# Kernel tuning notes

Measured on AMD Instinct MI355X. Metric: run time of the kernel, lower is better.

## Reference

```python
import jax, jax.numpy as jnp
import numpy as np

T, B, D = 2048, 2, 768
N, HD = 12, 64  # num_heads, head_dim; N*HD == D


def _rel_shift(s):
    # s: [I, J, B, N] -> Transformer-XL relative shift along J
    I, J, b, n = s.shape
    s = jnp.pad(s, ((0, 0), (1, 0), (0, 0), (0, 0)))  # [I, J+1, B, N]
    s = s.reshape(J + 1, I, b, n)[1:]                  # drop first row after transpose-view
    return s.reshape(I, J, b, n)


def setup_inputs() -> dict:
    key = jax.random.key(0)
    ks = jax.random.split(key, 8)
    x = jax.random.normal(ks[0], (T, B, D), dtype=jnp.float32)
    pos_encodings = jax.random.normal(ks[1], (T, D), dtype=jnp.float32)
    u_bias = jax.random.normal(ks[2], (N, HD), dtype=jnp.float32) * 0.02
    v_bias = jax.random.normal(ks[3], (N, HD), dtype=jnp.float32) * 0.02
    # causal mask: True = masked (j > i)
    attn_mask = jnp.triu(jnp.ones((T, T), dtype=bool), k=1)
    W_qkv = jax.random.normal(ks[4], (D, 3 * N * HD), dtype=jnp.float32) * 0.02
    W_pos = jax.random.normal(ks[5], (D, N * HD), dtype=jnp.float32) * 0.02
    W_out = jax.random.normal(ks[6], (N * HD, D), dtype=jnp.float32) * 0.02
    return {"x": x, "pos_encodings": pos_encodings, "u_bias": u_bias,
            "v_bias": v_bias, "W_qkv": W_qkv, "W_pos": W_pos,
            "W_out": W_out, "attn_mask": attn_mask}


def reference(x, pos_encodings, u_bias, v_bias, W_qkv, W_pos, W_out, attn_mask):
    tgt, bsz, dim = x.shape
    n, hd = u_bias.shape
    scale = 1.0 / (dim ** 0.5)  # NOTE: original scales by 1/sqrt(dim), not head_dim

    qkv = x @ W_qkv                                   # [T, B, 3*N*HD]
    q, k, v = jnp.split(qkv, 3, axis=-1)
    q = q.reshape(tgt, bsz, n, hd)
    k = k.reshape(tgt, bsz, n, hd)
    v = v.reshape(tgt, bsz, n, hd)
    pos = (pos_encodings @ W_pos).reshape(-1, n, hd)  # [P, N, HD]

    content_score = jnp.einsum('ibnd,jbnd->ijbn', q + u_bias, k)
    pos_score = jnp.einsum('ibnd,jnd->ijbn', q + v_bias, pos)
    pos_score = _rel_shift(pos_score)

    attn_score = (content_score + pos_score) * scale  # [T, S, B, N]
    attn_score = jnp.where(attn_mask[:, :, None, None], -jnp.inf, attn_score)
    attn = jax.nn.softmax(attn_score, axis=1)

    context = jnp.einsum('ijbn,jbnd->ibnd', attn, v)
    context = context.reshape(tgt, bsz, n * hd)
    return context @ W_out                            # [T, B, D]
```

## Files before the change

kernel.cpp:

```cpp
#include <hip/hip_runtime.h>
#include <math.h>

#define T_SEQ 2048
#define BSZ   2
#define DIM   768
#define NH    12
#define SCALE_L2 0.05205877f

typedef float f32x4 __attribute__((ext_vector_type(4)));
typedef __bf16 bf16x8 __attribute__((ext_vector_type(8)));
typedef unsigned int uint_t;
typedef unsigned short us16;

static __device__ __forceinline__ f32x4 mfma16(bf16x8 a, bf16x8 b, f32x4 c) {
    return __builtin_amdgcn_mfma_f32_16x16x32_bf16(a, b, c, 0, 0, 0);
}
static __device__ __forceinline__ us16 f2bf(float f) {
    uint_t u = __builtin_bit_cast(uint_t, f);
    u += 0x7fff + ((u >> 16) & 1);
    return (us16)(u >> 16);
}
static __device__ __forceinline__ us16 f2bf_up(float f) {
    return (us16)((__builtin_bit_cast(uint_t, f) + 0x8000u) >> 16);
}
static __device__ __forceinline__ float bf2f(us16 h) {
    return __builtin_bit_cast(float, (uint_t)h << 16);
}
static __device__ __forceinline__ bf16x8 ld_frag(const us16* p) {
    union { uint4 u; bf16x8 b; } x;
    x.u = *(const uint4*)p;
    return x.b;
}

typedef __attribute__((address_space(1))) const unsigned int guint;
typedef __attribute__((address_space(3))) unsigned int luint;
static __device__ __forceinline__ void glds16(const us16* g, us16* l) {
    __builtin_amdgcn_global_load_lds((guint*)g, (luint*)l, 16, 0, 0);
}

__constant__ int SLOT_IB[30] = {15,15,15, 14,14,14, 13,13, 12,12, 11,11,
                                10,10, 9,9, 8,8, 7,7, 6,6, 5, 4, 3,3, 2,2, 1, 0};
__constant__ int SLOT_C0[30] = {0,11,22, 0,10,20, 0,14, 0,13, 0,12,
                                0,11, 0,10, 0,14, 0,14, 0,12, 0, 0, 0,4, 0,3, 0, 0};
__constant__ int SLOT_C1[30] = {11,22,32, 10,20,30, 14,28, 13,26, 12,24,
                                11,22, 10,20, 14,18, 14,16, 12,14, 12, 10, 4,8, 3,6, 4, 2};
__constant__ int ORDER[30] = {6,7,16,18, 8,9, 10,11,20,22, 0,1,12,13,
                              2,3,4,5,14,15,23,
                              17,24,25,28, 26,27, 19,21,29};
__constant__ int CB_IB[12]   = {2,3,6,7,8,9,10,11,12,13,14,15};
__constant__ int CB_BASE[12] = {26,24,20,18,16,14,12,10,8,6,3,0};
__constant__ int CB_N[12]    = {2,2,2,2,2,2,2,2,2,2,3,3};

__global__ __launch_bounds__(256)
void cvt_all(const float* __restrict__ x, us16* __restrict__ xb, int n0,
             const float* __restrict__ pe, us16* __restrict__ peb, int n1,
             const float* __restrict__ w0, us16* __restrict__ o0,
             const float* __restrict__ w1, us16* __restrict__ o1,
             const float* __restrict__ w2, us16* __restrict__ o2) {
    const int bid = blockIdx.x;
    const int tid = threadIdx.x;
    if (bid < 1024) {
        int idx = bid * 256 + tid;
        int stride = 1024 * 256;
        int ntot = n0 + n1;
        for (int i = idx; i < ntot; i += stride) {
            const float4* src;
            ushort4* dst;
            if (i < n0) { src = (const float4*)x + i; dst = (ushort4*)xb + i; }
            else        { src = (const float4*)pe + (i - n0); dst = (ushort4*)peb + (i - n0); }
            float4 f = *src;
            ushort4 o;
            o.x = f2bf(f.x); o.y = f2bf(f.y); o.z = f2bf(f.z); o.w = f2bf(f.w);
            *dst = o;
        }
        return;
    }
    __shared__ us16 Ts[64][72];
    const int wb = bid - 1024;
    const float* in; us16* out; int C, bx, by;
    if (wb < 432)      { in = w0; out = o0; C = 2304; bx = wb % 36;        by = wb / 36; }
    else if (wb < 576) { in = w1; out = o1; C = 768;  bx = (wb - 432) % 12; by = (wb - 432) / 12; }
    else               { in = w2; out = o2; C = 768;  bx = (wb - 576) % 12; by = (wb - 576) / 12; }
    const int R = 768;
    const int c0 = bx * 64, r0 = by * 64;
    {
        const int r = tid >> 2, cq = (tid & 3) * 16;
        const float* src = in + (size_t)(r0 + r) * C + c0 + cq;
        #pragma unroll
        for (int i = 0; i < 4; ++i) {
            float4 f = *(const float4*)(src + i * 4);
            Ts[cq + i * 4 + 0][r] = f2bf(f.x);
            Ts[cq + i * 4 + 1][r] = f2bf(f.y);
            Ts[cq + i * 4 + 2][r] = f2bf(f.z);
            Ts[cq + i * 4 + 3][r] = f2bf(f.w);
        }
    }
    __syncthreads();
    {
        const int oc = tid >> 2, rq = (tid & 3) * 16;
        us16* dst = out + (size_t)(c0 + oc) * R + r0 + rq;
        *(uint4*)dst       = *(uint4*)&Ts[oc][rq];
        *(uint4*)(dst + 8) = *(uint4*)&Ts[oc][rq + 8];
    }
}

template <int BM, typename OutT>
static __device__ __forceinline__
void gemm_body(const us16* __restrict__ A, const us16* __restrict__ Bt,
               OutT* __restrict__ C, int N, int K, int m0, int n0,
               us16* As , us16* Bs ) {
    constexpr int MI   = BM / 32;
    constexpr int ABUF = BM * 32;
    const int tid  = threadIdx.x;
    const int lane = tid & 63;
    const int w    = tid >> 6;
    const int g    = lane >> 4;
    const int lm   = lane & 15;
    const int wm = (w >> 1) * (MI * 16), wn = (w & 1) * 64;

    const int nc0 = (w * 2 + 0) * 64 + lane;
    const int nc1 = (w * 2 + 1) * 64 + lane;
    const us16* bs0 = Bt + (size_t)(n0 + (nc0 >> 2)) * K + (nc0 & 3) * 8;
    const us16* bs1 = Bt + (size_t)(n0 + (nc1 >> 2)) * K + (nc1 & 3) * 8;

    const us16* as0;
    const us16* as1 = nullptr;
    if constexpr (BM == 128) {
        as0 = A + (size_t)(m0 + (nc0 >> 2)) * K + (nc0 & 3) * 8;
        as1 = A + (size_t)(m0 + (nc1 >> 2)) * K + (nc1 & 3) * 8;
    } else {
        const int nca = w * 64 + lane;
        as0 = A + (size_t)(m0 + (nca >> 2)) * K + (nca & 3) * 8;
    }

    f32x4 acc[MI][4];
    #pragma unroll
    for (int i = 0; i < MI; ++i)
        #pragma unroll
        for (int j = 0; j < 4; ++j) acc[i][j] = (f32x4){0.f, 0.f, 0.f, 0.f};

    auto STAGE = [&](int buf) {
        if constexpr (BM == 128) {
            glds16(as0, &As[buf * ABUF + (w * 2 + 0) * 512]);
            glds16(as1, &As[buf * ABUF + (w * 2 + 1) * 512]);
            as0 += 32; as1 += 32;
        } else {
            glds16(as0, &As[buf * ABUF + w * 512]);
            as0 += 32;
        }
        glds16(bs0, &Bs[buf * 4096 + (w * 2 + 0) * 512]);
        glds16(bs1, &Bs[buf * 4096 + (w * 2 + 1) * 512]);
        bs0 += 32; bs1 += 32;
    };
    auto COMPUTE = [&](int buf) {
        bf16x8 af[MI], bfr[4];
        #pragma unroll
        for (int mi = 0; mi < MI; ++mi)
            af[mi]  = ld_frag(&As[buf * ABUF + (wm + mi * 16 + lm) * 32 + g * 8]);
        #pragma unroll
        for (int ni = 0; ni < 4; ++ni)
            bfr[ni] = ld_frag(&Bs[buf * 4096 + (wn + ni * 16 + lm) * 32 + g * 8]);
        #pragma unroll
        for (int mi = 0; mi < MI; ++mi)
            #pragma unroll
            for (int ni = 0; ni < 4; ++ni)
                acc[mi][ni] = mfma16(af[mi], bfr[ni], acc[mi][ni]);
    };

    const int nsteps = K / 32;
    STAGE(0);
    __syncthreads();
    for (int it = 0; it < nsteps / 2; ++it) {
        STAGE(1);
        COMPUTE(0);
        __syncthreads();
        if (it * 2 + 2 < nsteps) STAGE(0);
        COMPUTE(1);
        __syncthreads();
    }

    #pragma unroll
    for (int mi = 0; mi < MI; ++mi) {
        #pragma unroll
        for (int reg = 0; reg < 4; ++reg) {
            int row = m0 + wm + mi * 16 + g * 4 + reg;
            OutT* crow = C + (size_t)row * N + n0 + wn + lm;
            #pragma unroll
            for (int ni = 0; ni < 4; ++ni) {
                float v = acc[mi][ni][reg];
                if constexpr (sizeof(OutT) == 2)
                    *(us16*)&crow[ni * 16] = f2bf(v);
                else
                    crow[ni * 16] = v;
            }
        }
    }
}

__global__ __launch_bounds__(256)
void gemm_dual(const us16* __restrict__ A0, const us16* __restrict__ B0, us16* __restrict__ C0,
               const us16* __restrict__ A1, const us16* __restrict__ B1, us16* __restrict__ C1) {
    __shared__ us16 As[2 * 128 * 32];
    __shared__ us16 Bs[2 * 128 * 32];
    const int bid = blockIdx.x;
    if (bid < 576) {
        gemm_body<128, us16>(A0, B0, C0, 2304, 768, (bid / 18) * 128, (bid % 18) * 128, As, Bs);
    } else {
        const int b = bid - 576;
        gemm_body<128, us16>(A1, B1, C1, 768, 768, (b / 6) * 128, (b % 6) * 128, As, Bs);
    }
}

__global__ __launch_bounds__(256)
void gemm_out(const us16* __restrict__ A, const us16* __restrict__ Bt,
              float* __restrict__ C) {
    __shared__ us16 As[2 * 64 * 32];
    __shared__ us16 Bs[2 * 128 * 32];
    gemm_body<64, float>(A, Bt, C, 768, 768, (int)blockIdx.y * 64, (int)blockIdx.x * 128, As, Bs);
}

__global__ __launch_bounds__(512, 4)
void attn_mfma(const us16* __restrict__ qkvb, const us16* __restrict__ posb,
               const float* __restrict__ u_bias, const float* __restrict__ v_bias,
               us16* __restrict__ ctx, float* __restrict__ pO, float* __restrict__ pML)
{
    __shared__ us16 Ks[64][72];
    __shared__ us16 Vt[80][72];
    __shared__ us16 Band[256][72];
    __shared__ us16 Ps[8][16][72];

    const int tid  = threadIdx.x;
    const int lane = tid & 63;
    const int w    = tid >> 6;
    const int g    = lane >> 4;
    const int lm   = lane & 15;

    const int flat = (int)blockIdx.y * 30 + (int)blockIdx.x;
    const int rank = flat / 24;
    const int y    = flat % 24;
    const int slot = ORDER[rank];

    const int ib = SLOT_IB[slot];
    const int c0 = SLOT_C0[slot], c1 = SLOT_C1[slot];
    const int i0 = ib * 128;
    const int n  = y % NH, b = y / NH;
    const int i_w0 = i0 + w * 16;
    const bool multi = !(ib == 0 || ib == 1 || ib == 4 || ib == 5);

    for (int idx = tid; idx < 576; idx += 512) {
        int r = idx / 36, c = (idx % 36) * 2;
        *(uint_t*)&Vt[64 + r][c] = 0x3F803F80u;
    }

    bf16x8 Qu[2], Qv[2];
    {
        const int qi = i_w0 + lm;
        const us16* qrow = qkvb + (size_t)(qi * BSZ + b) * 2304 + n * 64;
        #pragma unroll
        for (int ks = 0; ks < 2; ++ks) {
            const int h0 = ks * 32 + g * 8;
            union { uint4 u; us16 s[8]; } q;
            q.u = *(const uint4*)(qrow + h0);
            union { bf16x8 bv; us16 s[8]; } fu, fv;
            #pragma unroll
            for (int e = 0; e < 8; ++e) {
                float f  = bf2f(q.s[e]);
                fu.s[e] = f2bf((f + u_bias[n * 64 + h0 + e]) * SCALE_L2);
                fv.s[e] = f2bf((f + v_bias[n * 64 + h0 + e]) * SCALE_L2);
            }
            Qu[ks] = fu.bv; Qv[ks] = fv.bv;
        }
    }

    const int jr = tid >> 3, cc = (tid & 7) * 8;
    const int jp = tid & 31, hb = (tid >> 5) * 4;
    {
        const int j0 = c0 * 64;
        *(uint4*)&Ks[jr][cc] =
            *(const uint4*)(qkvb + (size_t)((j0 + jr) * BSZ + b) * 2304 + 768 + n * 64 + cc);
        const us16* v0 = qkvb + (size_t)((j0 + 2 * jp) * BSZ + b) * 2304 + 1536 + n * 64 + hb;
        union { uint2 u; us16 s[4]; } r0, r1;
        r0.u = *(const uint2*)v0;
        r1.u = *(const uint2*)(v0 + 2 * 2304);
        #pragma unroll
        for (int k = 0; k < 4; ++k)
            *(uint_t*)&Vt[hb + k][2 * jp] = (uint_t)r0.s[k] | ((uint_t)r1.s[k] << 16);
        const int t_min0 = T_SEQ - 128 - i0 + j0;
        #pragma unroll
        for (int pass = 0; pass < 3; ++pass) {
            int t = t_min0 + pass * 64 + jr;
            uint4 val = make_uint4(0u, 0u, 0u, 0u);
            if (t < T_SEQ)
                val = *(const uint4*)(posb + (size_t)t * DIM + n * 64 + cc);
            *(uint4*)&Band[t & 255][cc] = val;
        }
    }
    __syncthreads();

    f32x4 Oacc[5];
    #pragma unroll
    for (int hs = 0; hs < 5; ++hs) Oacc[hs] = (f32x4){0.f, 0.f, 0.f, 0.f};
    float m = -INFINITY;

    const int base_w = 112 - 16 * w;

    uint4 sK, sB;
    uint2 sV0, sV1;

    for (int jt = c0; jt < c1; ++jt) {
        const int j0 = jt * 64;
        const int t_min = T_SEQ - 128 - i0 + j0;
        const bool pf = (jt + 1 < c1);

        if (pf) {
            const int j0n = j0 + 64;
            sK = *(const uint4*)(qkvb + (size_t)((j0n + jr) * BSZ + b) * 2304 + 768 + n * 64 + cc);
            const us16* v0 = qkvb + (size_t)((j0n + 2 * jp) * BSZ + b) * 2304 + 1536 + n * 64 + hb;
            sV0 = *(const uint2*)v0;
            sV1 = *(const uint2*)(v0 + 2 * 2304);
            const int t_new = t_min + 192 + jr;
            sB = make_uint4(0u, 0u, 0u, 0u);
            if (t_new < T_SEQ)
                sB = *(const uint4*)(posb + (size_t)t_new * DIM + n * 64 + cc);
        }

        __builtin_amdgcn_s_setprio(1);
        f32x4 R[5];
        {
            const int rb = t_min + base_w + lm;
            #pragma unroll
            for (int gs = 0; gs < 5; ++gs) {
                const int row = (rb + gs * 16) & 255;
                f32x4 a = (f32x4){0.f, 0.f, 0.f, 0.f};
                a = mfma16(Qv[0], ld_frag(&Band[row][g * 8]), a);
                a = mfma16(Qv[1], ld_frag(&Band[row][32 + g * 8]), a);
                R[gs] = a;
            }
        }
        f32x4 S4[4];
        #pragma unroll
        for (int js = 0; js < 4; ++js) {
            f32x4 s4 = (f32x4){0.f, 0.f, 0.f, 0.f};
            s4 = mfma16(Qu[0], ld_frag(&Ks[js * 16 + lm][g * 8]), s4);
            s4 = mfma16(Qu[1], ld_frag(&Ks[js * 16 + lm][32 + g * 8]), s4);
            S4[js] = s4;
        }
        __builtin_amdgcn_s_setprio(0);

        float sv[4][4];
        if (j0 + 63 <= i_w0) {
            #pragma unroll
            for (int reg = 0; reg < 4; ++reg) {
                const int r   = g * 4 + reg;
                const int idx = lm + 15 - r;
                const int rot = (lane & 48) | (idx & 15);
                #pragma unroll
                for (int js = 0; js < 4; ++js) {
                    float va = __shfl(R[js][reg], rot);
                    float vb = __shfl(R[js + 1][reg], rot);
                    sv[js][reg] = S4[js][reg] + ((idx & 16) ? vb : va);
                }
            }
        } else {
            #pragma unroll
            for (int reg = 0; reg < 4; ++reg) {
                const int r   = g * 4 + reg;
                const int idx = lm + 15 - r;
                const int rot = (lane & 48) | (idx & 15);
                #pragma unroll
                for (int js = 0; js < 4; ++js) {
                    float va = __shfl(R[js][reg], rot);
                    float vb = __shfl(R[js + 1][reg], rot);
                    float rv = (idx & 16) ? vb : va;
                    int jg = j0 + js * 16 + lm;
                    sv[js][reg] = (jg <= i_w0 + r) ? (S4[js][reg] + rv) : -INFINITY;
                }
            }
        }

        float tm = sv[0][0];
        #pragma unroll
        for (int js = 0; js < 4; ++js)
            #pragma unroll
            for (int reg = 0; reg < 4; ++reg) tm = fmaxf(tm, sv[js][reg]);
        #pragma unroll
        for (int d = 1; d < 16; d <<= 1) tm = fmaxf(tm, __shfl_xor(tm, d));
        if (tm > m + 8.0f) {
            float alpha = __builtin_amdgcn_exp2f(m - tm);
            m = tm;
            #pragma unroll
            for (int hs = 0; hs < 5; ++hs)
                #pragma unroll
                for (int reg = 0; reg < 4; ++reg) Oacc[hs][reg] *= alpha;
        }

        #pragma unroll
        for (int reg = 0; reg < 4; ++reg) {
            const int r = g * 4 + reg;
            #pragma unroll
            for (int js = 0; js < 4; ++js) {
                float p = __builtin_amdgcn_exp2f(sv[js][reg] - m);
                Ps[w][r][js * 16 + lm] = f2bf_up(p);
            }
        }

        __builtin_amdgcn_s_setprio(1);
        #pragma unroll
        for (int ks = 0; ks < 2; ++ks) {
            bf16x8 Pf = ld_frag(&Ps[w][lm][ks * 32 + g * 8]);
            #pragma unroll
            for (int hs = 0; hs < 5; ++hs) {
                bf16x8 Vf = ld_frag(&Vt[hs * 16 + lm][ks * 32 + g * 8]);
                Oacc[hs] = mfma16(Pf, Vf, Oacc[hs]);
            }
        }
        __builtin_amdgcn_s_setprio(0);

        if (pf) {
            __syncthreads();
            *(uint4*)&Ks[jr][cc] = sK;
            union { uint2 u; us16 s[4]; } r0, r1;
            r0.u = sV0; r1.u = sV1;
            #pragma unroll
            for (int k = 0; k < 4; ++k)
                *(uint_t*)&Vt[hb + k][2 * jp] = (uint_t)r0.s[k] | ((uint_t)r1.s[k] << 16);
            const int t_new = t_min + 192 + jr;
            *(uint4*)&Band[t_new & 255][cc] = sB;
            __syncthreads();
        }
    }

    if (multi) {
        const size_t pbase = ((size_t)y * 30 + slot) * 128;
        #pragma unroll
        for (int reg = 0; reg < 4; ++reg) {
            const int r = w * 16 + g * 4 + reg;
            float* orow = pO + (pbase + r) * 64 + lm;
            #pragma unroll
            for (int hs = 0; hs < 4; ++hs) orow[hs * 16] = Oacc[hs][reg];
            if (lm == 0) {
                pML[(pbase + r) * 2 + 0] = m;
                pML[(pbase + r) * 2 + 1] = Oacc[4][reg];
            }
        }
    } else {
        #pragma unroll
        for (int reg = 0; reg < 4; ++reg) {
            const int ig = i_w0 + g * 4 + reg;
            float inv = 1.0f / Oacc[4][reg];
            us16* crow = ctx + (size_t)(ig * BSZ + b) * DIM + n * 64;
            #pragma unroll
            for (int hs = 0; hs < 4; ++hs)
                crow[hs * 16 + lm] = f2bf(Oacc[hs][reg] * inv);
        }
    }
}

__global__ __launch_bounds__(256)
void attn_combine(const float* __restrict__ pO, const float* __restrict__ pML,
                  us16* __restrict__ ctx) {
    const int ib = CB_IB[blockIdx.x];
    const int y  = blockIdx.y;
    const int n = y % NH, b = y / NH;
    const int base = CB_BASE[blockIdx.x], nc = CB_N[blockIdx.x];
    const int tid = threadIdx.x;
    const int r = tid >> 1, half = (tid & 1) * 32;

    float mc[4], lc[4], sc[4];
    float mstar = -INFINITY;
    #pragma unroll
    for (int c = 0; c < 4; ++c) {
        mc[c] = -INFINITY; lc[c] = 0.f;
        if (c < nc) {
            const float* ml = pML + ((size_t)(y * 30 + base + c) * 128 + r) * 2;
            mc[c] = ml[0]; lc[c] = ml[1];
        }
        mstar = fmaxf(mstar, mc[c]);
    }
    float lstar = 0.f;
    #pragma unroll
    for (int c = 0; c < 4; ++c) {
        sc[c] = (c < nc) ? __builtin_amdgcn_exp2f(mc[c] - mstar) : 0.f;
        lstar += sc[c] * lc[c];
    }
    const float inv = 1.0f / lstar;

    f32x4 acc[8];
    #pragma unroll
    for (int k = 0; k < 8; ++k) acc[k] = (f32x4){0.f, 0.f, 0.f, 0.f};
    #pragma unroll
    for (int c = 0; c < 4; ++c) {
        if (c < nc) {
            const f32x4* src = (const f32x4*)(pO + ((size_t)(y * 30 + base + c) * 128 + r) * 64 + half);
            float s = sc[c];
            #pragma unroll
            for (int k = 0; k < 8; ++k) acc[k] += src[k] * s;
        }
    }
    const int ig = ib * 128 + r;
    us16* crow = ctx + (size_t)(ig * BSZ + b) * DIM + n * 64 + half;
    #pragma unroll
    for (int k = 0; k < 8; ++k) {
        us16 q[4];
        #pragma unroll
        for (int e = 0; e < 4; ++e) q[e] = f2bf(acc[k][e] * inv);
        *(uint2*)&crow[k * 4] = *(uint2*)q;
    }
}

extern "C" void kernel_launch(void* const* d_in, const int* in_sizes, int n_in,
                              void* d_out, int out_size, void* d_ws, size_t ws_size,
                              hipStream_t stream) {
    const float* x      = (const float*)d_in[0];
    const float* pe     = (const float*)d_in[1];
    const float* u_bias = (const float*)d_in[2];
    const float* v_bias = (const float*)d_in[3];
    const float* W_qkv  = (const float*)d_in[4];
    const float* W_pos  = (const float*)d_in[5];
    const float* W_out  = (const float*)d_in[6];
    float* out = (float*)d_out;

    char* ws = (char*)d_ws;
    us16*  qkvb  = (us16*)(ws);
    us16*  posb  = (us16*)(ws + 18874368);
    us16*  ctxb  = (us16*)(ws + 22020096);
    us16*  Woutb = (us16*)(ws + 28311552);
    float* pML   = (float*)(ws + 29491200);
    float* pO    = (float*)(ws + 30228480);
    us16*  xb    = (us16*)(ws + 30228480);
    us16*  peb   = (us16*)(ws + 36519936);
    us16*  Wqkvb = (us16*)(ws + 39665664);
    us16*  Wposb = (us16*)(ws + 43204608);

    dim3 blk(256);
    cvt_all<<<1744, blk, 0, stream>>>(x, xb, 4096 * 768 / 4, pe, peb, 2048 * 768 / 4,
                                      W_qkv, Wqkvb, W_pos, Wposb, W_out, Woutb);
    gemm_dual<<<672, blk, 0, stream>>>(xb, Wqkvb, qkvb, peb, Wposb, posb);
    attn_mfma<<<dim3(30, 24), dim3(512), 0, stream>>>(qkvb, posb, u_bias, v_bias, ctxb, pO, pML);
    attn_combine<<<dim3(12, 24), blk, 0, stream>>>(pO, pML, ctxb);
    gemm_out<<<dim3(768 / 128, 4096 / 64), blk, 0, stream>>>(ctxb, Woutb, out);
}
```

Measured before the change: 134.0 us.

## Rebalance causal attention split into uniform 8-chunk slots across 40 work items

Replaces the uneven 30-slot split of query blocks over key chunks with 40 slots of at most 8 key chunks each. All query blocks from 4 upward are split and merged in the combine kernel, with its indexing, partial-buffer stride and workspace offsets updated to match. The launch order puts longer slots first. The aim is to cut tail imbalance and fill the GPU better, at the cost of more partial writes and combine work.

```diff
diff --git a/kernel.cpp b/kernel.cpp
--- a/kernel.cpp
+++ b/kernel.cpp
@@ -38,18 +38,20 @@
     __builtin_amdgcn_global_load_lds((guint*)g, (luint*)l, 16, 0, 0);
 }
 
-__constant__ int SLOT_IB[30] = {15,15,15, 14,14,14, 13,13, 12,12, 11,11,
-                                10,10, 9,9, 8,8, 7,7, 6,6, 5, 4, 3,3, 2,2, 1, 0};
-__constant__ int SLOT_C0[30] = {0,11,22, 0,10,20, 0,14, 0,13, 0,12,
-                                0,11, 0,10, 0,14, 0,14, 0,12, 0, 0, 0,4, 0,3, 0, 0};
-__constant__ int SLOT_C1[30] = {11,22,32, 10,20,30, 14,28, 13,26, 12,24,
-                                11,22, 10,20, 14,18, 14,16, 12,14, 12, 10, 4,8, 3,6, 4, 2};
-__constant__ int ORDER[30] = {6,7,16,18, 8,9, 10,11,20,22, 0,1,12,13,
-                              2,3,4,5,14,15,23,
-                              17,24,25,28, 26,27, 19,21,29};
-__constant__ int CB_IB[12]   = {2,3,6,7,8,9,10,11,12,13,14,15};
-__constant__ int CB_BASE[12] = {26,24,20,18,16,14,12,10,8,6,3,0};
-__constant__ int CB_N[12]    = {2,2,2,2,2,2,2,2,2,2,3,3};
+__constant__ int SLOT_IB[40] = {15,15,15,15, 14,14,14,14, 13,13,13,13, 12,12,12,12,
+                                11,11,11, 10,10,10, 9,9,9, 8,8,8,
+                                7,7, 6,6, 5,5, 4,4, 3, 2, 1, 0};
+__constant__ int SLOT_C0[40] = {0,8,16,24, 0,8,16,24, 0,8,16,24, 0,8,16,24,
+                                0,8,16, 0,8,16, 0,8,16, 0,8,16,
+                                0,8, 0,8, 0,8, 0,8, 0, 0, 0, 0};
+__constant__ int SLOT_C1[40] = {8,16,24,32, 8,16,24,30, 8,16,24,28, 8,16,24,26,
+                                8,16,24, 8,16,22, 8,16,20, 8,16,18,
+                                8,16, 8,14, 8,12, 8,10, 8, 6, 4, 2};
+__constant__ int ORDER[40] = {0,1,2,3,4,5,6,8,9,10,12,13,14,16,17,18,19,20,22,23,
+                              25,26,28,29,30,32,34,36,
+                              7,21,31,37,  11,24,33,38,  15,27,35,39};
+__constant__ int CB_BASE[12] = {34,32,30,28, 25,22,19,16, 12,8,4,0};
+__constant__ int CB_N[12]    = {2,2,2,2, 3,3,3,3, 4,4,4,4};
 
 __global__ __launch_bounds__(256)
 void cvt_all(const float* __restrict__ x, us16* __restrict__ xb, int n0,
@@ -235,7 +237,7 @@
     const int g    = lane >> 4;
     const int lm   = lane & 15;
 
-    const int flat = (int)blockIdx.y * 30 + (int)blockIdx.x;
+    const int flat = (int)blockIdx.y * 40 + (int)blockIdx.x;
     const int rank = flat / 24;
     const int y    = flat % 24;
     const int slot = ORDER[rank];
@@ -245,7 +247,7 @@
     const int i0 = ib * 128;
     const int n  = y % NH, b = y / NH;
     const int i_w0 = i0 + w * 16;
-    const bool multi = !(ib == 0 || ib == 1 || ib == 4 || ib == 5);
+    const bool multi = (ib >= 4);
 
     for (int idx = tid; idx < 576; idx += 512) {
         int r = idx / 36, c = (idx % 36) * 2;
@@ -431,7 +433,7 @@
     }
 
     if (multi) {
-        const size_t pbase = ((size_t)y * 30 + slot) * 128;
+        const size_t pbase = ((size_t)y * 36 + slot) * 128;
         #pragma unroll
         for (int reg = 0; reg < 4; ++reg) {
             const int r = w * 16 + g * 4 + reg;
@@ -459,7 +461,7 @@
 __global__ __launch_bounds__(256)
 void attn_combine(const float* __restrict__ pO, const float* __restrict__ pML,
                   us16* __restrict__ ctx) {
-    const int ib = CB_IB[blockIdx.x];
+    const int ib = 4 + blockIdx.x;
     const int y  = blockIdx.y;
     const int n = y % NH, b = y / NH;
     const int base = CB_BASE[blockIdx.x], nc = CB_N[blockIdx.x];
@@ -472,7 +474,7 @@
     for (int c = 0; c < 4; ++c) {
         mc[c] = -INFINITY; lc[c] = 0.f;
         if (c < nc) {
-            const float* ml = pML + ((size_t)(y * 30 + base + c) * 128 + r) * 2;
+            const float* ml = pML + ((size_t)(y * 36 + base + c) * 128 + r) * 2;
             mc[c] = ml[0]; lc[c] = ml[1];
         }
         mstar = fmaxf(mstar, mc[c]);
@@ -491,7 +493,7 @@
     #pragma unroll
     for (int c = 0; c < 4; ++c) {
         if (c < nc) {
-            const f32x4* src = (const f32x4*)(pO + ((size_t)(y * 30 + base + c) * 128 + r) * 64 + half);
+            const f32x4* src = (const f32x4*)(pO + ((size_t)(y * 36 + base + c) * 128 + r) * 64 + half);
             float s = sc[c];
             #pragma unroll
             for (int k = 0; k < 8; ++k) acc[k] += src[k] * s;
@@ -526,17 +528,17 @@
     us16*  ctxb  = (us16*)(ws + 22020096);
     us16*  Woutb = (us16*)(ws + 28311552);
     float* pML   = (float*)(ws + 29491200);
-    float* pO    = (float*)(ws + 30228480);
-    us16*  xb    = (us16*)(ws + 30228480);
-    us16*  peb   = (us16*)(ws + 36519936);
-    us16*  Wqkvb = (us16*)(ws + 39665664);
-    us16*  Wposb = (us16*)(ws + 43204608);
+    float* pO    = (float*)(ws + 30375936);
+    us16*  xb    = (us16*)(ws + 30375936);
+    us16*  peb   = (us16*)(ws + 36667392);
+    us16*  Wqkvb = (us16*)(ws + 39813120);
+    us16*  Wposb = (us16*)(ws + 43352064);
 
     dim3 blk(256);
     cvt_all<<<1744, blk, 0, stream>>>(x, xb, 4096 * 768 / 4, pe, peb, 2048 * 768 / 4,
                                       W_qkv, Wqkvb, W_pos, Wposb, W_out, Woutb);
     gemm_dual<<<672, blk, 0, stream>>>(xb, Wqkvb, qkvb, peb, Wposb, posb);
-    attn_mfma<<<dim3(30, 24), dim3(512), 0, stream>>>(qkvb, posb, u_bias, v_bias, ctxb, pO, pML);
+    attn_mfma<<<dim3(40, 24), dim3(512), 0, stream>>>(qkvb, posb, u_bias, v_bias, ctxb, pO, pML);
     attn_combine<<<dim3(12, 24), blk, 0, stream>>>(pO, pML, ctxb);
     gemm_out<<<dim3(768 / 128, 4096 / 64), blk, 0, stream>>>(ctxb, Woutb, out);
 }
```

New measurement: 134.3 us. About the same (+0.2%).
